# Kernel tuning notes

Hardware: AMD Instinct MI355X
Metric: run time of the kernel (lower is better)

## Reference

```python
import jax, jax.numpy as jnp
import numpy as np
import math

B, T, N, DS, A = 8, 64, 16, 128, 32
C, H, L = 1024, 16, 8
BLOCK = 64
MAX_TS = 1024


def _ln(x, w, b, eps=1e-5):
    m = x.mean(-1, keepdims=True)
    v = ((x - m) ** 2).mean(-1, keepdims=True)
    return (x - m) / jnp.sqrt(v + eps) * w + b


def _gelu(x):
    # tanh-approx GELU exactly as in the torch module
    return 0.5 * x * (1.0 + jnp.tanh(math.sqrt(2.0 / math.pi) * (x + 0.044715 * x ** 3)))


def setup_inputs() -> dict:
    key = jax.random.key(0)
    ks = jax.random.split(key, 24)
    w = lambda k, shape: (jax.random.normal(k, shape, jnp.float32) * 0.02)
    inp = {
        "states": jax.random.normal(ks[0], (B, T, N, DS), jnp.float32),
        "actions": jax.random.normal(ks[1], (B, T, N, A), jnp.float32),
        "timesteps": jax.random.randint(ks[2], (B, T), 0, MAX_TS),
        "pos_emb": w(ks[3], (2 * BLOCK, C)),
        "global_pos_emb": w(ks[4], (MAX_TS + 1, C)),
        "se_W": w(ks[5], (DS, C)), "se_b": jnp.zeros((C,), jnp.float32),
        "ae_W": w(ks[6], (A, C)), "ae_b": jnp.zeros((C,), jnp.float32),
        "ln1_w": jnp.ones((L, C), jnp.float32), "ln1_b": jnp.zeros((L, C), jnp.float32),
        "Wq": w(ks[7], (L, C, C)), "bq": jnp.zeros((L, C), jnp.float32),
        "Wk": w(ks[8], (L, C, C)), "bk": jnp.zeros((L, C), jnp.float32),
        "Wv": w(ks[9], (L, C, C)), "bv": jnp.zeros((L, C), jnp.float32),
        "Wp": w(ks[10], (L, C, C)), "bp": jnp.zeros((L, C), jnp.float32),
        "ln2_w": jnp.ones((L, C), jnp.float32), "ln2_b": jnp.zeros((L, C), jnp.float32),
        "W1": w(ks[11], (L, C, 4 * C)), "b1": jnp.zeros((L, 4 * C), jnp.float32),
        "W2": w(ks[12], (L, 4 * C, C)), "b2": jnp.zeros((L, C), jnp.float32),
        "lnf_w": jnp.ones((C,), jnp.float32), "lnf_b": jnp.zeros((C,), jnp.float32),
        "head_W": w(ks[13], (C, A)),
    }
    return inp


def _forward(states, actions, timesteps, pos_emb, global_pos_emb, se_W, se_b, ae_W, ae_b,
             ln1_w, ln1_b, Wq, bq, Wk, bk, Wv, bv, Wp, bp, ln2_w, ln2_b,
             W1, b1, W2, b2, lnf_w, lnf_b, head_W):
    BN = B * N
    S = 2 * T
    d = C // H
    st = states.transpose(0, 2, 1, 3).reshape(BN, T, DS)
    ac = actions.transpose(0, 2, 1, 3).reshape(BN, T, A)
    ts = jnp.broadcast_to(timesteps[:, None, :], (B, N, T)).reshape(BN, T)

    se = st @ se_W + se_b            # [BN, T, C]
    ae = ac @ ae_W + ae_b            # [BN, T, C]
    tok = jnp.stack([se, ae], axis=2).reshape(BN, S, C)  # interleave s,a

    gpe = global_pos_emb[ts]                              # [BN, T, C]
    pos = pos_emb[:S] + jnp.repeat(gpe, 2, axis=1)        # [BN, S, C]
    x = tok + pos

    causal = jnp.tril(jnp.ones((S, S), dtype=bool))

    def block(x, p):
        l1w, l1b, wq, bq_, wk, bk_, wv, bv_, wp, bp_, l2w, l2b, w1, b1_, w2, b2_ = p
        h = _ln(x, l1w, l1b)
        q = (h @ wq + bq_).reshape(BN, S, H, d).transpose(0, 2, 1, 3)
        k = (h @ wk + bk_).reshape(BN, S, H, d).transpose(0, 2, 1, 3)
        v = (h @ wv + bv_).reshape(BN, S, H, d).transpose(0, 2, 1, 3)
        att = jnp.einsum('bhqd,bhkd->bhqk', q, k) * (1.0 / math.sqrt(d))
        att = jnp.where(causal, att, -jnp.inf)
        att = jax.nn.softmax(att, axis=-1)
        y = jnp.einsum('bhqk,bhkd->bhqd', att, v).transpose(0, 2, 1, 3).reshape(BN, S, C)
        x = x + y @ wp + bp_
        h2 = _ln(x, l2w, l2b)
        x = x + _gelu(h2 @ w1 + b1_) @ w2 + b2_
        return x, None

    x, _ = jax.lax.scan(block, x, (ln1_w, ln1_b, Wq, bq, Wk, bk, Wv, bv, Wp, bp,
                                   ln2_w, ln2_b, W1, b1, W2, b2))
    x = _ln(x, lnf_w, lnf_b)
    logits = x @ head_W                                   # [BN, S, A]
    preds = logits[:, -2, :].reshape(B, N, A)
    return preds[:, None, :, :]                           # [B, 1, N, A]


def reference(states, actions, timesteps, pos_emb, global_pos_emb, se_W, se_b, ae_W, ae_b,
              ln1_w, ln1_b, Wq, bq, Wk, bk, Wv, bv, Wp, bp, ln2_w, ln2_b,
              W1, b1, W2, b2, lnf_w, lnf_b, head_W):
    return _forward(states, actions, timesteps, pos_emb, global_pos_emb, se_W, se_b, ae_W, ae_b,
                    ln1_w, ln1_b, Wq, bq, Wk, bk, Wv, bv, Wp, bp, ln2_w, ln2_b,
                    W1, b1, W2, b2, lnf_w, lnf_b, head_W)
```

## Files before the change

### kernel.cpp

```cpp
#include <hip/hip_runtime.h>
#include <math.h>


typedef float  float4v __attribute__((ext_vector_type(4)));
typedef short  short8  __attribute__((ext_vector_type(8)));

__device__ inline unsigned short f2b(float f) {
    unsigned int u = __float_as_uint(f);
    u += 0x7fffu + ((u >> 16) & 1u);
    return (unsigned short)(u >> 16);
}
__device__ inline float gelu_f(float v) {
    return 0.5f * v * (1.0f + tanhf(0.7978845608028654f * (v + 0.044715f * v * v * v)));
}
__device__ inline float4v mfma16(short8 a, short8 b, float4v c) {
    return __builtin_amdgcn_mfma_f32_16x16x32_bf16(a, b, c, 0, 0, 0);
}
#define GLOAD_LDS16(gp, lp)                                                 \
    __builtin_amdgcn_global_load_lds(                                       \
        (__attribute__((address_space(1))) void*)(gp),                      \
        (__attribute__((address_space(3))) void*)(lp), 16, 0, 0)

__global__ __launch_bounds__(256) void embed_kernel(
    const float* __restrict__ states, const float* __restrict__ actions,
    const int* __restrict__ timesteps, const float* __restrict__ pos_emb,
    const float* __restrict__ gpe_tab, const float* __restrict__ seW,
    const float* __restrict__ seb, const float* __restrict__ aeW,
    const float* __restrict__ aeb, float* __restrict__ x)
{
    const int c0 = blockIdx.x * 128;
    const int m0 = blockIdx.y * 32;
    const int bn = m0 >> 7;
    const int b  = bn >> 4, n = bn & 15;
    const int s_base = m0 & 127;
    const int tid = threadIdx.x;

    __shared__ float st[16][128];
    __shared__ float ac[16][32];
    for (int idx = tid; idx < 16 * 128; idx += 256) {
        int rr = idx >> 7, ds = idx & 127;
        int t = (s_base >> 1) + rr;
        st[rr][ds] = states[(((size_t)b * 64 + t) * 16 + n) * 128 + ds];
    }
    for (int idx = tid; idx < 16 * 32; idx += 256) {
        int rr = idx >> 5, a = idx & 31;
        int t = (s_base >> 1) + rr;
        ac[rr][a] = actions[(((size_t)b * 64 + t) * 16 + n) * 32 + a];
    }
    __syncthreads();

    const int half = tid >> 7;
    const int sub  = tid & 127;
    const int cg   = sub & 31;
    const int rg   = sub >> 5;

    float acc[4][4];
    for (int i = 0; i < 4; i++) for (int j = 0; j < 4; j++) acc[i][j] = 0.f;

    if (half == 0) {
        for (int kk = 0; kk < 128; kk++) {
            float4 w4 = *(const float4*)&seW[(size_t)kk * 1024 + c0 + cg * 4];
            for (int r4 = 0; r4 < 4; r4++) {
                float sv = st[rg * 4 + r4][kk];
                acc[r4][0] += sv * w4.x; acc[r4][1] += sv * w4.y;
                acc[r4][2] += sv * w4.z; acc[r4][3] += sv * w4.w;
            }
        }
    } else {
        for (int kk = 0; kk < 32; kk++) {
            float4 w4 = *(const float4*)&aeW[(size_t)kk * 1024 + c0 + cg * 4];
            for (int r4 = 0; r4 < 4; r4++) {
                float sv = ac[rg * 4 + r4][kk];
                acc[r4][0] += sv * w4.x; acc[r4][1] += sv * w4.y;
                acc[r4][2] += sv * w4.z; acc[r4][3] += sv * w4.w;
            }
        }
    }
    const float* bias = half ? aeb : seb;
    float4 b4 = *(const float4*)&bias[c0 + cg * 4];
    for (int r4 = 0; r4 < 4; r4++) {
        int rr = rg * 4 + r4;
        int s  = s_base + rr * 2 + half;
        int t  = (s_base >> 1) + rr;
        int m  = bn * 128 + s;
        int ts = timesteps[b * 64 + t];
        float4 p4 = *(const float4*)&pos_emb[(size_t)s * 1024 + c0 + cg * 4];
        float4 g4 = *(const float4*)&gpe_tab[(size_t)ts * 1024 + c0 + cg * 4];
        float4 o;
        o.x = acc[r4][0] + b4.x + p4.x + g4.x;
        o.y = acc[r4][1] + b4.y + p4.y + g4.y;
        o.z = acc[r4][2] + b4.z + p4.z + g4.z;
        o.w = acc[r4][3] + b4.w + p4.w + g4.w;
        *(float4*)&x[(size_t)m * 1024 + c0 + cg * 4] = o;
    }
}

__global__ __launch_bounds__(256) void transpose_kernel(
    const float* __restrict__ src, unsigned short* __restrict__ dst, int K, int N)
{
    __shared__ float tile[32][65];
    const int n0 = blockIdx.x * 32, k0 = blockIdx.y * 64;
    const int tid = threadIdx.x;
    const int nl = tid & 31, kl = tid >> 5;
    for (int p = 0; p < 8; p++)
        tile[nl][p * 8 + kl] = src[(size_t)(k0 + p * 8 + kl) * N + n0 + nl];
    __syncthreads();
    const int n2 = tid >> 3, kseg = tid & 7;
    unsigned short o8[8];
    for (int u = 0; u < 8; u++) o8[u] = f2b(tile[n2][kseg * 8 + u]);
    *(uint4*)&dst[(size_t)(n0 + n2) * K + k0 + kseg * 8] = *(uint4*)o8;
}

__global__ __launch_bounds__(256) void ln_kernel(
    const float* __restrict__ x, const float* __restrict__ w,
    const float* __restrict__ b, unsigned short* __restrict__ out)
{
    const int tid = threadIdx.x;
    const int row = blockIdx.x * 2 + (tid >> 7);
    const int sub = tid & 127;
    const float* xr = x + (size_t)row * 1024 + sub * 8;
    float4 a = *(const float4*)xr;
    float4 c = *(const float4*)(xr + 4);
    float s  = a.x + a.y + a.z + a.w + c.x + c.y + c.z + c.w;
    float s2 = a.x*a.x + a.y*a.y + a.z*a.z + a.w*a.w
             + c.x*c.x + c.y*c.y + c.z*c.z + c.w*c.w;
    for (int o = 32; o > 0; o >>= 1) { s += __shfl_down(s, o); s2 += __shfl_down(s2, o); }
    __shared__ float ls[4], ls2[4];
    if ((tid & 63) == 0) { ls[tid >> 6] = s; ls2[tid >> 6] = s2; }
    __syncthreads();
    const int wp = (tid >> 7) * 2;
    s  = ls[wp] + ls[wp + 1];
    s2 = ls2[wp] + ls2[wp + 1];
    float mean = s * (1.f / 1024.f);
    float var  = s2 * (1.f / 1024.f) - mean * mean;
    float inv  = rsqrtf(var + 1e-5f);
    float4 wa = *(const float4*)&w[sub * 8];
    float4 wc = *(const float4*)&w[sub * 8 + 4];
    float4 ba = *(const float4*)&b[sub * 8];
    float4 bc = *(const float4*)&b[sub * 8 + 4];
    unsigned short o8[8];
    o8[0] = f2b((a.x - mean) * inv * wa.x + ba.x);
    o8[1] = f2b((a.y - mean) * inv * wa.y + ba.y);
    o8[2] = f2b((a.z - mean) * inv * wa.z + ba.z);
    o8[3] = f2b((a.w - mean) * inv * wa.w + ba.w);
    o8[4] = f2b((c.x - mean) * inv * wc.x + bc.x);
    o8[5] = f2b((c.y - mean) * inv * wc.y + bc.y);
    o8[6] = f2b((c.z - mean) * inv * wc.z + bc.z);
    o8[7] = f2b((c.w - mean) * inv * wc.w + bc.w);
    *(uint4*)&out[(size_t)row * 1024 + sub * 8] = *(uint4*)o8;
}

template <int MODE>
__global__ __launch_bounds__(256) void gemm_kernel(
    const unsigned short* __restrict__ A, const unsigned short* __restrict__ Bt,
    const float* __restrict__ bias, const float* __restrict__ resid,
    void* __restrict__ outp, int M, int N, int K)
{
    __shared__ unsigned short As[128][32];
    __shared__ unsigned short Bs[128][32];
    __shared__ __align__(16) char Osmem[32768];
    const int tid = threadIdx.x;
    const int w  = tid >> 6, l = tid & 63;
    const int wr = w >> 1, wc = w & 1;
    const int qd = l >> 4, r = l & 15;
    const int m0 = blockIdx.y * 128, n0 = blockIdx.x * 128;

    const unsigned short* Ab = A  + (size_t)m0 * K;
    const unsigned short* Bb = Bt + (size_t)n0 * K;

    float4v acc[4][4];
    float4v zero = {0.f, 0.f, 0.f, 0.f};
    for (int i = 0; i < 4; i++) for (int j = 0; j < 4; j++) acc[i][j] = zero;

    const int ra0 = tid >> 2,         ca0 = (tid & 3) * 8;
    const int ra1 = (tid + 256) >> 2, ca1 = ((tid + 256) & 3) * 8;

    for (int k0 = 0; k0 < K; k0 += 32) {
        GLOAD_LDS16(Ab + (size_t)ra0 * K + k0 + ca0, &As[ra0][ca0]);
        GLOAD_LDS16(Ab + (size_t)ra1 * K + k0 + ca1, &As[ra1][ca1]);
        GLOAD_LDS16(Bb + (size_t)ra0 * K + k0 + ca0, &Bs[ra0][ca0]);
        GLOAD_LDS16(Bb + (size_t)ra1 * K + k0 + ca1, &Bs[ra1][ca1]);
        __syncthreads();
        short8 af[4], bfv[4];
        for (int i = 0; i < 4; i++) af[i]  = *(const short8*)&As[wr * 64 + i * 16 + r][qd * 8];
        for (int j = 0; j < 4; j++) bfv[j] = *(const short8*)&Bs[wc * 64 + j * 16 + r][qd * 8];
        for (int i = 0; i < 4; i++)
            for (int j = 0; j < 4; j++)
                acc[i][j] = mfma16(af[i], bfv[j], acc[i][j]);
        __syncthreads();
    }

    if (MODE != 2) {
        unsigned short (*Ob)[128] = (unsigned short (*)[128])Osmem;
        for (int i = 0; i < 4; i++) {
            const int rl = wr * 64 + i * 16 + qd * 4;
            for (int j = 0; j < 4; j++) {
                const int cl = wc * 64 + j * 16 + r;
                const float bv = bias[n0 + cl];
                for (int t4 = 0; t4 < 4; t4++) {
                    float v = acc[i][j][t4] + bv;
                    if (MODE == 1) v = gelu_f(v);
                    Ob[rl + t4][cl] = f2b(v);
                }
            }
        }
        __syncthreads();
        unsigned short* op = (unsigned short*)outp;
        for (int it = 0; it < 8; it++) {
            const int idx = it * 256 + tid;
            const int rl = idx >> 4, seg = idx & 15;
            *(uint4*)&op[(size_t)(m0 + rl) * N + n0 + seg * 8] = *(uint4*)&Ob[rl][seg * 8];
        }
    } else {
        float (*Of)[128] = (float (*)[128])Osmem;
        float* op = (float*)outp;
        for (int p = 0; p < 2; p++) {
            if (wr == p) {
                for (int i = 0; i < 4; i++) {
                    const int rl = i * 16 + qd * 4;
                    for (int j = 0; j < 4; j++) {
                        const int cl = wc * 64 + j * 16 + r;
                        const float bv = bias[n0 + cl];
                        for (int t4 = 0; t4 < 4; t4++)
                            Of[rl + t4][cl] = acc[i][j][t4] + bv;
                    }
                }
            }
            __syncthreads();
            for (int it = 0; it < 8; it++) {
                const int idx = it * 256 + tid;
                const int rl = idx >> 5, c4 = (idx & 31) * 4;
                const size_t go = (size_t)(m0 + p * 64 + rl) * N + n0 + c4;
                float4 rv = *(const float4*)&resid[go];
                float4 ov = *(float4*)&Of[rl][c4];
                ov.x += rv.x; ov.y += rv.y; ov.z += rv.z; ov.w += rv.w;
                *(float4*)&op[go] = ov;
            }
            __syncthreads();
        }
    }
}

__global__ __launch_bounds__(256) void attn_kernel(
    const unsigned short* __restrict__ qm, const unsigned short* __restrict__ km,
    const unsigned short* __restrict__ vm, unsigned short* __restrict__ ym)
{
    const int bn = blockIdx.x >> 4, hd = blockIdx.x & 15;
    __shared__ unsigned short QK[2][128][64];
    __shared__ unsigned short Vt[64][128];
    __shared__ float Sc[128][128];
    __shared__ float rsum[128];
    unsigned short (*Pb)[128] = (unsigned short (*)[128])QK;

    const int tid = threadIdx.x;
    const int w = tid >> 6, l = tid & 63, qd = l >> 4, r = l & 15;
    const size_t base = ((size_t)bn * 128) * 1024 + hd * 64;

    for (int idx = tid; idx < 1024; idx += 256) {
        int row = idx >> 3, seg = idx & 7;
        *(uint4*)&QK[0][row][seg * 8] = *(const uint4*)&qm[base + (size_t)row * 1024 + seg * 8];
        *(uint4*)&QK[1][row][seg * 8] = *(const uint4*)&km[base + (size_t)row * 1024 + seg * 8];
    }
    for (int idx = tid; idx < 8192; idx += 256) {
        int s = idx >> 6, d = idx & 63;
        Vt[d][s] = vm[base + (size_t)s * 1024 + d];
    }
    __syncthreads();

    for (int im = 0; im < 2; im++) {
        const int i = w * 2 + im;
        float4v acc[8];
        float4v zero = {0.f, 0.f, 0.f, 0.f};
        for (int j = 0; j < 8; j++) acc[j] = zero;
        for (int k0 = 0; k0 < 64; k0 += 32) {
            short8 af = *(const short8*)&QK[0][i * 16 + r][k0 + qd * 8];
            for (int j = 0; j < 8; j++) {
                short8 bf = *(const short8*)&QK[1][j * 16 + r][k0 + qd * 8];
                acc[j] = mfma16(af, bf, acc[j]);
            }
        }
        for (int j = 0; j < 8; j++)
            for (int t4 = 0; t4 < 4; t4++)
                Sc[i * 16 + qd * 4 + t4][j * 16 + r] = acc[j][t4] * 0.125f;
    }
    __syncthreads();

    if (tid < 128) {
        const int s = tid;
        float mx = -1e30f;
        for (int j = 0; j <= s; j++) mx = fmaxf(mx, Sc[s][j]);
        float sum = 0.f;
        for (int j = 0; j <= s; j++) {
            float e = __expf(Sc[s][j] - mx);
            sum += e;
            Pb[s][j] = f2b(e);
        }
        for (int j = s + 1; j < 128; j++) Pb[s][j] = 0;
        rsum[s] = 1.f / sum;
    }
    __syncthreads();

    float4v acc2[2][4];
    {
        float4v zero = {0.f, 0.f, 0.f, 0.f};
        for (int im = 0; im < 2; im++) for (int j = 0; j < 4; j++) acc2[im][j] = zero;
    }
    for (int im = 0; im < 2; im++) {
        const int i = w * 2 + im;
        for (int k0 = 0; k0 < 128; k0 += 32) {
            short8 af = *(const short8*)&Pb[i * 16 + r][k0 + qd * 8];
            for (int j = 0; j < 4; j++) {
                short8 bf = *(const short8*)&Vt[j * 16 + r][k0 + qd * 8];
                acc2[im][j] = mfma16(af, bf, acc2[im][j]);
            }
        }
    }
    __syncthreads();
    unsigned short (*Ys)[64] = (unsigned short (*)[64])Vt;
    for (int im = 0; im < 2; im++) {
        const int i = w * 2 + im;
        for (int j = 0; j < 4; j++)
            for (int t4 = 0; t4 < 4; t4++) {
                const int srow = i * 16 + qd * 4 + t4;
                Ys[srow][j * 16 + r] = f2b(acc2[im][j][t4] * rsum[srow]);
            }
    }
    __syncthreads();
    for (int it = 0; it < 4; it++) {
        const int idx = it * 256 + tid;
        const int row = idx >> 3, seg = idx & 7;
        *(uint4*)&ym[base + (size_t)row * 1024 + seg * 8] = *(uint4*)&Ys[row][seg * 8];
    }
}

__global__ __launch_bounds__(256) void final_kernel(
    const float* __restrict__ x, const float* __restrict__ lnw,
    const float* __restrict__ lnb, const float* __restrict__ headW,
    float* __restrict__ out)
{
    const int bn = blockIdx.x;
    const int tid = threadIdx.x;
    const float* xr = x + ((size_t)bn * 128 + 126) * 1024;
    float4 v = *(const float4*)&xr[tid * 4];
    float s  = v.x + v.y + v.z + v.w;
    float s2 = v.x * v.x + v.y * v.y + v.z * v.z + v.w * v.w;
    for (int o = 32; o > 0; o >>= 1) { s += __shfl_down(s, o); s2 += __shfl_down(s2, o); }
    __shared__ float ls[4], ls2[4];
    if ((tid & 63) == 0) { ls[tid >> 6] = s; ls2[tid >> 6] = s2; }
    __syncthreads();
    s  = ls[0] + ls[1] + ls[2] + ls[3];
    s2 = ls2[0] + ls2[1] + ls2[2] + ls2[3];
    float mean = s * (1.f / 1024.f);
    float var  = s2 * (1.f / 1024.f) - mean * mean;
    float inv  = rsqrtf(var + 1e-5f);
    __shared__ float hf[1024];
    float4 wv = *(const float4*)&lnw[tid * 4];
    float4 bv = *(const float4*)&lnb[tid * 4];
    hf[tid * 4 + 0] = (v.x - mean) * inv * wv.x + bv.x;
    hf[tid * 4 + 1] = (v.y - mean) * inv * wv.y + bv.y;
    hf[tid * 4 + 2] = (v.z - mean) * inv * wv.z + bv.z;
    hf[tid * 4 + 3] = (v.w - mean) * inv * wv.w + bv.w;
    __syncthreads();
    const int a = tid & 31, part = tid >> 5;
    float sum = 0.f;
    for (int c = part * 128; c < (part + 1) * 128; c++)
        sum += hf[c] * headW[(size_t)c * 32 + a];
    __shared__ float red[256];
    red[tid] = sum;
    __syncthreads();
    if (part == 0) {
        float tot = 0.f;
        for (int p = 0; p < 8; p++) tot += red[p * 32 + a];
        out[(size_t)bn * 32 + a] = tot;
    }
}

extern "C" void kernel_launch(void* const* d_in, const int* in_sizes, int n_in,
                              void* d_out, int out_size, void* d_ws, size_t ws_size,
                              hipStream_t stream)
{
    const float* states    = (const float*)d_in[0];
    const float* actions   = (const float*)d_in[1];
    const int*   timesteps = (const int*)  d_in[2];
    const float* pos_emb   = (const float*)d_in[3];
    const float* gpe_tab   = (const float*)d_in[4];
    const float* seW  = (const float*)d_in[5];
    const float* seb  = (const float*)d_in[6];
    const float* aeW  = (const float*)d_in[7];
    const float* aeb  = (const float*)d_in[8];
    const float* ln1w = (const float*)d_in[9];
    const float* ln1b = (const float*)d_in[10];
    const float* Wq = (const float*)d_in[11];
    const float* bq = (const float*)d_in[12];
    const float* Wk = (const float*)d_in[13];
    const float* bk = (const float*)d_in[14];
    const float* Wv = (const float*)d_in[15];
    const float* bv = (const float*)d_in[16];
    const float* Wp = (const float*)d_in[17];
    const float* bp = (const float*)d_in[18];
    const float* ln2w = (const float*)d_in[19];
    const float* ln2b = (const float*)d_in[20];
    const float* W1 = (const float*)d_in[21];
    const float* b1 = (const float*)d_in[22];
    const float* W2 = (const float*)d_in[23];
    const float* b2 = (const float*)d_in[24];
    const float* lnfw  = (const float*)d_in[25];
    const float* lnfb  = (const float*)d_in[26];
    const float* headW = (const float*)d_in[27];

    char* ws = (char*)d_ws;
    const size_t MB = 1024 * 1024;
    float*          x   = (float*)ws;
    unsigned short* h   = (unsigned short*)(ws + 64 * MB);
    unsigned short* qb  = (unsigned short*)(ws + 96 * MB);
    unsigned short* kb  = (unsigned short*)(ws + 128 * MB);
    unsigned short* vb  = (unsigned short*)(ws + 160 * MB);
    unsigned short* yb  = (unsigned short*)(ws + 192 * MB);
    unsigned short* ub  = (unsigned short*)(ws + 96 * MB);
    unsigned short* wqT = (unsigned short*)(ws + 224 * MB);
    unsigned short* wkT = (unsigned short*)(ws + 226 * MB);
    unsigned short* wvT = (unsigned short*)(ws + 228 * MB);
    unsigned short* wpT = (unsigned short*)(ws + 230 * MB);
    unsigned short* w1T = (unsigned short*)(ws + 232 * MB);
    unsigned short* w2T = (unsigned short*)(ws + 240 * MB);

    embed_kernel<<<dim3(8, 512), 256, 0, stream>>>(
        states, actions, timesteps, pos_emb, gpe_tab, seW, seb, aeW, aeb, x);

    for (int lyr = 0; lyr < 8; lyr++) {
        const size_t oC  = (size_t)lyr * 1024 * 1024;
        const size_t oC4 = (size_t)lyr * 1024 * 4096;
        transpose_kernel<<<dim3(32, 16),  256, 0, stream>>>(Wq + oC,  wqT, 1024, 1024);
        transpose_kernel<<<dim3(32, 16),  256, 0, stream>>>(Wk + oC,  wkT, 1024, 1024);
        transpose_kernel<<<dim3(32, 16),  256, 0, stream>>>(Wv + oC,  wvT, 1024, 1024);
        transpose_kernel<<<dim3(32, 16),  256, 0, stream>>>(Wp + oC,  wpT, 1024, 1024);
        transpose_kernel<<<dim3(128, 16), 256, 0, stream>>>(W1 + oC4, w1T, 1024, 4096);
        transpose_kernel<<<dim3(32, 64),  256, 0, stream>>>(W2 + oC4, w2T, 4096, 1024);

        ln_kernel<<<8192, 256, 0, stream>>>(x, ln1w + lyr * 1024, ln1b + lyr * 1024, h);
        gemm_kernel<0><<<dim3(8, 128), 256, 0, stream>>>(h, wqT, bq + lyr * 1024, nullptr, qb, 16384, 1024, 1024);
        gemm_kernel<0><<<dim3(8, 128), 256, 0, stream>>>(h, wkT, bk + lyr * 1024, nullptr, kb, 16384, 1024, 1024);
        gemm_kernel<0><<<dim3(8, 128), 256, 0, stream>>>(h, wvT, bv + lyr * 1024, nullptr, vb, 16384, 1024, 1024);
        attn_kernel<<<2048, 256, 0, stream>>>(qb, kb, vb, yb);
        gemm_kernel<2><<<dim3(8, 128), 256, 0, stream>>>(yb, wpT, bp + lyr * 1024, x, x, 16384, 1024, 1024);
        ln_kernel<<<8192, 256, 0, stream>>>(x, ln2w + lyr * 1024, ln2b + lyr * 1024, h);
        gemm_kernel<1><<<dim3(32, 128), 256, 0, stream>>>(h, w1T, b1 + lyr * 4096, nullptr, ub, 16384, 4096, 1024);
        gemm_kernel<2><<<dim3(8, 128), 256, 0, stream>>>(ub, w2T, b2 + lyr * 1024, x, x, 16384, 1024, 4096);
    }

    final_kernel<<<128, 256, 0, stream>>>(x, lnfw, lnfb, headW, (float*)d_out);
}
```

Baseline: 7.753 ms.

## Prune last layer to needed rows, swizzle LDS, parallelize attention softmax

In the final layer only row 126 of each sequence feeds the output, so the projection, LN2 and MLP GEMMs now run on those 128 rows via strided views instead of all 16384 rows. GEMM and attention kernels gain XOR-swizzled shared-memory layouts to cut bank conflicts. The attention softmax now uses all 256 threads with vectorized reads, and the V transpose goes through LDS with vector loads. GELU is rewritten in an exp-based sigmoid form that is algebraically equivalent to the tanh version. The main risks are the added index arithmetic and the strided last-layer launches being correct.

```diff
diff --git a/kernel.cpp b/kernel.cpp
--- a/kernel.cpp
+++ b/kernel.cpp
@@ -11,7 +11,8 @@
     return (unsigned short)(u >> 16);
 }
 __device__ inline float gelu_f(float v) {
-    return 0.5f * v * (1.0f + tanhf(0.7978845608028654f * (v + 0.044715f * v * v * v)));
+    float z2 = 1.5957691216057308f * v + 0.07135481282377437f * v * v * v;
+    return v - v / (__expf(z2) + 1.0f);
 }
 __device__ inline float4v mfma16(short8 a, short8 b, float4v c) {
     return __builtin_amdgcn_mfma_f32_16x16x32_bf16(a, b, c, 0, 0, 0);
@@ -112,13 +113,13 @@
 }
 
 __global__ __launch_bounds__(256) void ln_kernel(
-    const float* __restrict__ x, const float* __restrict__ w,
+    const float* __restrict__ x, long xrs, const float* __restrict__ w,
     const float* __restrict__ b, unsigned short* __restrict__ out)
 {
     const int tid = threadIdx.x;
     const int row = blockIdx.x * 2 + (tid >> 7);
     const int sub = tid & 127;
-    const float* xr = x + (size_t)row * 1024 + sub * 8;
+    const float* xr = x + (size_t)row * xrs + sub * 8;
     float4 a = *(const float4*)xr;
     float4 c = *(const float4*)(xr + 4);
     float s  = a.x + a.y + a.z + a.w + c.x + c.y + c.z + c.w;
@@ -154,36 +155,36 @@
 __global__ __launch_bounds__(256) void gemm_kernel(
     const unsigned short* __restrict__ A, const unsigned short* __restrict__ Bt,
     const float* __restrict__ bias, const float* __restrict__ resid,
-    void* __restrict__ outp, int M, int N, int K)
-{
-    __shared__ unsigned short As[128][32];
-    __shared__ unsigned short Bs[128][32];
-    __shared__ __align__(16) char Osmem[32768];
+    void* __restrict__ outp, int N, int K, long Ars, long Ors)
+{
+    __shared__ __align__(16) char smem[32768];
+    unsigned short* As = (unsigned short*)smem;
+    unsigned short* Bs = (unsigned short*)(smem + 16384);
     const int tid = threadIdx.x;
     const int w  = tid >> 6, l = tid & 63;
     const int wr = w >> 1, wc = w & 1;
     const int qd = l >> 4, r = l & 15;
     const int m0 = blockIdx.y * 128, n0 = blockIdx.x * 128;
 
-    const unsigned short* Ab = A  + (size_t)m0 * K;
+    const unsigned short* Ab = A  + (size_t)m0 * Ars;
     const unsigned short* Bb = Bt + (size_t)n0 * K;
 
     float4v acc[4][4];
     float4v zero = {0.f, 0.f, 0.f, 0.f};
     for (int i = 0; i < 4; i++) for (int j = 0; j < 4; j++) acc[i][j] = zero;
 
-    const int ra0 = tid >> 2,         ca0 = (tid & 3) * 8;
-    const int ra1 = (tid + 256) >> 2, ca1 = ((tid + 256) & 3) * 8;
+    const int ra0 = tid >> 2,  ca = (tid & 3) * 8;
+    const int ra1 = ra0 + 64;
 
     for (int k0 = 0; k0 < K; k0 += 32) {
-        GLOAD_LDS16(Ab + (size_t)ra0 * K + k0 + ca0, &As[ra0][ca0]);
-        GLOAD_LDS16(Ab + (size_t)ra1 * K + k0 + ca1, &As[ra1][ca1]);
-        GLOAD_LDS16(Bb + (size_t)ra0 * K + k0 + ca0, &Bs[ra0][ca0]);
-        GLOAD_LDS16(Bb + (size_t)ra1 * K + k0 + ca1, &Bs[ra1][ca1]);
+        GLOAD_LDS16(Ab + (size_t)ra0 * Ars + k0 + ca, As + tid * 8);
+        GLOAD_LDS16(Ab + (size_t)ra1 * Ars + k0 + ca, As + (256 + tid) * 8);
+        GLOAD_LDS16(Bb + (size_t)ra0 * K   + k0 + ca, Bs + tid * 8);
+        GLOAD_LDS16(Bb + (size_t)ra1 * K   + k0 + ca, Bs + (256 + tid) * 8);
         __syncthreads();
         short8 af[4], bfv[4];
-        for (int i = 0; i < 4; i++) af[i]  = *(const short8*)&As[wr * 64 + i * 16 + r][qd * 8];
-        for (int j = 0; j < 4; j++) bfv[j] = *(const short8*)&Bs[wc * 64 + j * 16 + r][qd * 8];
+        for (int i = 0; i < 4; i++) af[i]  = *(const short8*)(As + (wr*64 + i*16 + r)*32 + qd*8);
+        for (int j = 0; j < 4; j++) bfv[j] = *(const short8*)(Bs + (wc*64 + j*16 + r)*32 + qd*8);
         for (int i = 0; i < 4; i++)
             for (int j = 0; j < 4; j++)
                 acc[i][j] = mfma16(af[i], bfv[j], acc[i][j]);
@@ -191,16 +192,16 @@
     }
 
     if (MODE != 2) {
-        unsigned short (*Ob)[128] = (unsigned short (*)[128])Osmem;
+        unsigned short* Ob = (unsigned short*)smem;
         for (int i = 0; i < 4; i++) {
-            const int rl = wr * 64 + i * 16 + qd * 4;
             for (int j = 0; j < 4; j++) {
                 const int cl = wc * 64 + j * 16 + r;
                 const float bv = bias[n0 + cl];
                 for (int t4 = 0; t4 < 4; t4++) {
+                    const int rl = wr * 64 + i * 16 + qd * 4 + t4;
                     float v = acc[i][j][t4] + bv;
                     if (MODE == 1) v = gelu_f(v);
-                    Ob[rl + t4][cl] = f2b(v);
+                    Ob[rl * 128 + (((cl >> 3) ^ (rl & 15)) << 3) + (cl & 7)] = f2b(v);
                 }
             }
         }
@@ -209,30 +210,33 @@
         for (int it = 0; it < 8; it++) {
             const int idx = it * 256 + tid;
             const int rl = idx >> 4, seg = idx & 15;
-            *(uint4*)&op[(size_t)(m0 + rl) * N + n0 + seg * 8] = *(uint4*)&Ob[rl][seg * 8];
+            *(uint4*)&op[(size_t)(m0 + rl) * Ors + n0 + seg * 8] =
+                *(uint4*)&Ob[rl * 128 + ((seg ^ (rl & 15)) << 3)];
         }
     } else {
-        float (*Of)[128] = (float (*)[128])Osmem;
+        float* Of = (float*)smem;
         float* op = (float*)outp;
         for (int p = 0; p < 2; p++) {
             if (wr == p) {
                 for (int i = 0; i < 4; i++) {
-                    const int rl = i * 16 + qd * 4;
                     for (int j = 0; j < 4; j++) {
                         const int cl = wc * 64 + j * 16 + r;
                         const float bv = bias[n0 + cl];
-                        for (int t4 = 0; t4 < 4; t4++)
-                            Of[rl + t4][cl] = acc[i][j][t4] + bv;
+                        for (int t4 = 0; t4 < 4; t4++) {
+                            const int lr = i * 16 + qd * 4 + t4;
+                            Of[lr * 128 + (((cl >> 2) ^ (lr & 31)) << 2) + (cl & 3)] =
+                                acc[i][j][t4] + bv;
+                        }
                     }
                 }
             }
             __syncthreads();
             for (int it = 0; it < 8; it++) {
                 const int idx = it * 256 + tid;
-                const int rl = idx >> 5, c4 = (idx & 31) * 4;
-                const size_t go = (size_t)(m0 + p * 64 + rl) * N + n0 + c4;
+                const int lr = idx >> 5, c4 = idx & 31;
+                const size_t go = (size_t)(m0 + p * 64 + lr) * Ors + n0 + c4 * 4;
                 float4 rv = *(const float4*)&resid[go];
-                float4 ov = *(float4*)&Of[rl][c4];
+                float4 ov = *(const float4*)&Of[lr * 128 + ((c4 ^ (lr & 31)) << 2)];
                 ov.x += rv.x; ov.y += rv.y; ov.z += rv.z; ov.w += rv.w;
                 *(float4*)&op[go] = ov;
             }
@@ -246,90 +250,139 @@
     const unsigned short* __restrict__ vm, unsigned short* __restrict__ ym)
 {
     const int bn = blockIdx.x >> 4, hd = blockIdx.x & 15;
-    __shared__ unsigned short QK[2][128][64];
-    __shared__ unsigned short Vt[64][128];
-    __shared__ float Sc[128][128];
-    __shared__ float rsum[128];
-    unsigned short (*Pb)[128] = (unsigned short (*)[128])QK;
+    __shared__ __align__(16) unsigned short QK[2][128 * 64];
+    __shared__ __align__(16) unsigned short Vt[64 * 128];
+    __shared__ __align__(16) float Sc[128 * 128];
+    __shared__ float pmax[2][128], psum[2][128], rsum[128];
 
     const int tid = threadIdx.x;
     const int w = tid >> 6, l = tid & 63, qd = l >> 4, r = l & 15;
-    const size_t base = ((size_t)bn * 128) * 1024 + hd * 64;
-
+    const size_t base = ((size_t)bn * 128) * 1024 + (size_t)hd * 64;
+
+    unsigned short* Vs = (unsigned short*)Sc;
     for (int idx = tid; idx < 1024; idx += 256) {
         int row = idx >> 3, seg = idx & 7;
-        *(uint4*)&QK[0][row][seg * 8] = *(const uint4*)&qm[base + (size_t)row * 1024 + seg * 8];
-        *(uint4*)&QK[1][row][seg * 8] = *(const uint4*)&km[base + (size_t)row * 1024 + seg * 8];
-    }
-    for (int idx = tid; idx < 8192; idx += 256) {
-        int s = idx >> 6, d = idx & 63;
-        Vt[d][s] = vm[base + (size_t)s * 1024 + d];
-    }
-    __syncthreads();
-
+        int sw = (seg ^ (row & 7)) << 3;
+        *(uint4*)&QK[0][row * 64 + sw] = *(const uint4*)&qm[base + (size_t)row * 1024 + seg * 8];
+        *(uint4*)&QK[1][row * 64 + sw] = *(const uint4*)&km[base + (size_t)row * 1024 + seg * 8];
+        *(uint4*)&Vs[row * 64 + seg * 8] = *(const uint4*)&vm[base + (size_t)row * 1024 + seg * 8];
+    }
+    __syncthreads();
+
+    for (int idx = tid; idx < 1024; idx += 256) {
+        int d = idx & 63, sg = idx >> 6;
+        unsigned short tmp[8];
+        for (int u = 0; u < 8; u++) tmp[u] = Vs[(sg * 8 + u) * 64 + d];
+        *(uint4*)&Vt[d * 128 + ((sg ^ (d & 15)) << 3)] = *(uint4*)tmp;
+    }
+
+    float4v accS[2][8];
+    { float4v z = {0,0,0,0}; for (int a = 0; a < 2; a++) for (int j = 0; j < 8; j++) accS[a][j] = z; }
     for (int im = 0; im < 2; im++) {
         const int i = w * 2 + im;
-        float4v acc[8];
-        float4v zero = {0.f, 0.f, 0.f, 0.f};
-        for (int j = 0; j < 8; j++) acc[j] = zero;
+        const int rowA = i * 16 + r;
         for (int k0 = 0; k0 < 64; k0 += 32) {
-            short8 af = *(const short8*)&QK[0][i * 16 + r][k0 + qd * 8];
+            short8 af = *(const short8*)&QK[0][rowA * 64 + ((((k0 >> 3) + qd) ^ (rowA & 7)) << 3)];
             for (int j = 0; j < 8; j++) {
-                short8 bf = *(const short8*)&QK[1][j * 16 + r][k0 + qd * 8];
-                acc[j] = mfma16(af, bf, acc[j]);
-            }
-        }
-        for (int j = 0; j < 8; j++)
-            for (int t4 = 0; t4 < 4; t4++)
-                Sc[i * 16 + qd * 4 + t4][j * 16 + r] = acc[j][t4] * 0.125f;
-    }
-    __syncthreads();
-
-    if (tid < 128) {
-        const int s = tid;
-        float mx = -1e30f;
-        for (int j = 0; j <= s; j++) mx = fmaxf(mx, Sc[s][j]);
-        float sum = 0.f;
-        for (int j = 0; j <= s; j++) {
-            float e = __expf(Sc[s][j] - mx);
-            sum += e;
-            Pb[s][j] = f2b(e);
-        }
-        for (int j = s + 1; j < 128; j++) Pb[s][j] = 0;
-        rsum[s] = 1.f / sum;
-    }
-    __syncthreads();
-
-    float4v acc2[2][4];
-    {
-        float4v zero = {0.f, 0.f, 0.f, 0.f};
-        for (int im = 0; im < 2; im++) for (int j = 0; j < 4; j++) acc2[im][j] = zero;
-    }
+                const int rowB = j * 16 + r;
+                short8 bf = *(const short8*)&QK[1][rowB * 64 + ((((k0 >> 3) + qd) ^ (rowB & 7)) << 3)];
+                accS[im][j] = mfma16(af, bf, accS[im][j]);
+            }
+        }
+    }
+    __syncthreads();
+
     for (int im = 0; im < 2; im++) {
         const int i = w * 2 + im;
+        for (int j = 0; j < 8; j++)
+            for (int t4 = 0; t4 < 4; t4++) {
+                const int row = i * 16 + qd * 4 + t4;
+                const int col = j * 16 + r;
+                Sc[row * 128 + (((col >> 2) ^ (row & 31)) << 2) + (col & 3)] =
+                    accS[im][j][t4] * 0.125f;
+            }
+    }
+    __syncthreads();
+
+    {
+        const int s = tid & 127, half = tid >> 7;
+        float mx = -1e30f;
+        for (int g = half * 16; g < half * 16 + 16; g++) {
+            if (4 * g > s) break;
+            float4 v4 = *(const float4*)&Sc[s * 128 + ((g ^ (s & 31)) << 2)];
+            mx = fmaxf(mx, v4.x);
+            if (4 * g + 1 <= s) mx = fmaxf(mx, v4.y);
+            if (4 * g + 2 <= s) mx = fmaxf(mx, v4.z);
+            if (4 * g + 3 <= s) mx = fmaxf(mx, v4.w);
+        }
+        pmax[half][s] = mx;
+    }
+    __syncthreads();
+    {
+        const int s = tid & 127, half = tid >> 7;
+        const float mx = fmaxf(pmax[0][s], pmax[1][s]);
+        unsigned short* Pb = &QK[0][0];
+        float sum = 0.f;
+        for (int gg = half * 8; gg < half * 8 + 8; gg++) {
+            unsigned short o8[8] = {0, 0, 0, 0, 0, 0, 0, 0};
+            const int c0 = gg * 8;
+            if (c0 <= s) {
+                float4 a4 = *(const float4*)&Sc[s * 128 + (((2 * gg) ^ (s & 31)) << 2)];
+                float4 b4 = *(const float4*)&Sc[s * 128 + (((2 * gg + 1) ^ (s & 31)) << 2)];
+                float e;
+                e = __expf(a4.x - mx);                sum += e; o8[0] = f2b(e);
+                if (c0 + 1 <= s) { e = __expf(a4.y - mx); sum += e; o8[1] = f2b(e); }
+                if (c0 + 2 <= s) { e = __expf(a4.z - mx); sum += e; o8[2] = f2b(e); }
+                if (c0 + 3 <= s) { e = __expf(a4.w - mx); sum += e; o8[3] = f2b(e); }
+                if (c0 + 4 <= s) { e = __expf(b4.x - mx); sum += e; o8[4] = f2b(e); }
+                if (c0 + 5 <= s) { e = __expf(b4.y - mx); sum += e; o8[5] = f2b(e); }
+                if (c0 + 6 <= s) { e = __expf(b4.z - mx); sum += e; o8[6] = f2b(e); }
+                if (c0 + 7 <= s) { e = __expf(b4.w - mx); sum += e; o8[7] = f2b(e); }
+            }
+            *(uint4*)&Pb[s * 128 + ((gg ^ (s & 15)) << 3)] = *(uint4*)o8;
+        }
+        psum[half][s] = sum;
+    }
+    __syncthreads();
+    if (tid < 128) rsum[tid] = 1.f / (psum[0][tid] + psum[1][tid]);
+
+    const unsigned short* Pb = &QK[0][0];
+    float4v accO[2][4];
+    { float4v z = {0,0,0,0}; for (int a = 0; a < 2; a++) for (int j = 0; j < 4; j++) accO[a][j] = z; }
+    for (int im = 0; im < 2; im++) {
+        const int i = w * 2 + im;
+        const int rowA = i * 16 + r;
         for (int k0 = 0; k0 < 128; k0 += 32) {
-            short8 af = *(const short8*)&Pb[i * 16 + r][k0 + qd * 8];
+            short8 af = *(const short8*)&Pb[rowA * 128 + ((((k0 >> 3) + qd) ^ (rowA & 15)) << 3)];
             for (int j = 0; j < 4; j++) {
-                short8 bf = *(const short8*)&Vt[j * 16 + r][k0 + qd * 8];
-                acc2[im][j] = mfma16(af, bf, acc2[im][j]);
-            }
-        }
-    }
-    __syncthreads();
-    unsigned short (*Ys)[64] = (unsigned short (*)[64])Vt;
+                const int rowB = j * 16 + r;
+                short8 bf = *(const short8*)&Vt[rowB * 128 + ((((k0 >> 3) + qd) ^ (rowB & 15)) << 3)];
+                accO[im][j] = mfma16(af, bf, accO[im][j]);
+            }
+        }
+    }
+    __syncthreads();
+
+    float* Ys = Sc;
     for (int im = 0; im < 2; im++) {
         const int i = w * 2 + im;
         for (int j = 0; j < 4; j++)
             for (int t4 = 0; t4 < 4; t4++) {
-                const int srow = i * 16 + qd * 4 + t4;
-                Ys[srow][j * 16 + r] = f2b(acc2[im][j][t4] * rsum[srow]);
-            }
-    }
-    __syncthreads();
-    for (int it = 0; it < 4; it++) {
-        const int idx = it * 256 + tid;
-        const int row = idx >> 3, seg = idx & 7;
-        *(uint4*)&ym[base + (size_t)row * 1024 + seg * 8] = *(uint4*)&Ys[row][seg * 8];
+                const int row = i * 16 + qd * 4 + t4;
+                const int col = j * 16 + r;
+                Ys[row * 64 + (((col >> 2) ^ (row & 15)) << 2) + (col & 3)] =
+                    accO[im][j][t4] * rsum[row];
+            }
+    }
+    __syncthreads();
+    for (int idx = tid; idx < 1024; idx += 256) {
+        const int row = idx >> 3, gg = idx & 7;
+        float4 a4 = *(const float4*)&Ys[row * 64 + (((2 * gg) ^ (row & 15)) << 2)];
+        float4 b4 = *(const float4*)&Ys[row * 64 + (((2 * gg + 1) ^ (row & 15)) << 2)];
+        unsigned short o8[8];
+        o8[0] = f2b(a4.x); o8[1] = f2b(a4.y); o8[2] = f2b(a4.z); o8[3] = f2b(a4.w);
+        o8[4] = f2b(b4.x); o8[5] = f2b(b4.y); o8[6] = f2b(b4.z); o8[7] = f2b(b4.w);
+        *(uint4*)&ym[base + (size_t)row * 1024 + gg * 8] = *(uint4*)o8;
     }
 }
 
@@ -427,7 +480,11 @@
     embed_kernel<<<dim3(8, 512), 256, 0, stream>>>(
         states, actions, timesteps, pos_emb, gpe_tab, seW, seb, aeW, aeb, x);
 
+    const long G = 128L * 1024L;
+    float* xg = x + 126 * 1024;
+
     for (int lyr = 0; lyr < 8; lyr++) {
+        const bool last = (lyr == 7);
         const size_t oC  = (size_t)lyr * 1024 * 1024;
         const size_t oC4 = (size_t)lyr * 1024 * 4096;
         transpose_kernel<<<dim3(32, 16),  256, 0, stream>>>(Wq + oC,  wqT, 1024, 1024);
@@ -437,15 +494,23 @@
         transpose_kernel<<<dim3(128, 16), 256, 0, stream>>>(W1 + oC4, w1T, 1024, 4096);
         transpose_kernel<<<dim3(32, 64),  256, 0, stream>>>(W2 + oC4, w2T, 4096, 1024);
 
-        ln_kernel<<<8192, 256, 0, stream>>>(x, ln1w + lyr * 1024, ln1b + lyr * 1024, h);
-        gemm_kernel<0><<<dim3(8, 128), 256, 0, stream>>>(h, wqT, bq + lyr * 1024, nullptr, qb, 16384, 1024, 1024);
-        gemm_kernel<0><<<dim3(8, 128), 256, 0, stream>>>(h, wkT, bk + lyr * 1024, nullptr, kb, 16384, 1024, 1024);
-        gemm_kernel<0><<<dim3(8, 128), 256, 0, stream>>>(h, wvT, bv + lyr * 1024, nullptr, vb, 16384, 1024, 1024);
+        ln_kernel<<<8192, 256, 0, stream>>>(x, 1024L, ln1w + lyr * 1024, ln1b + lyr * 1024, h);
+        gemm_kernel<0><<<dim3(8, 128), 256, 0, stream>>>(h, wqT, bq + lyr * 1024, nullptr, qb, 1024, 1024, 1024L, 1024L);
+        gemm_kernel<0><<<dim3(8, 128), 256, 0, stream>>>(h, wkT, bk + lyr * 1024, nullptr, kb, 1024, 1024, 1024L, 1024L);
+        gemm_kernel<0><<<dim3(8, 128), 256, 0, stream>>>(h, wvT, bv + lyr * 1024, nullptr, vb, 1024, 1024, 1024L, 1024L);
         attn_kernel<<<2048, 256, 0, stream>>>(qb, kb, vb, yb);
-        gemm_kernel<2><<<dim3(8, 128), 256, 0, stream>>>(yb, wpT, bp + lyr * 1024, x, x, 16384, 1024, 1024);
-        ln_kernel<<<8192, 256, 0, stream>>>(x, ln2w + lyr * 1024, ln2b + lyr * 1024, h);
-        gemm_kernel<1><<<dim3(32, 128), 256, 0, stream>>>(h, w1T, b1 + lyr * 4096, nullptr, ub, 16384, 4096, 1024);
-        gemm_kernel<2><<<dim3(8, 128), 256, 0, stream>>>(ub, w2T, b2 + lyr * 1024, x, x, 16384, 1024, 4096);
+
+        if (!last) {
+            gemm_kernel<2><<<dim3(8, 128), 256, 0, stream>>>(yb, wpT, bp + lyr * 1024, x, x, 1024, 1024, 1024L, 1024L);
+            ln_kernel<<<8192, 256, 0, stream>>>(x, 1024L, ln2w + lyr * 1024, ln2b + lyr * 1024, h);
+            gemm_kernel<1><<<dim3(32, 128), 256, 0, stream>>>(h, w1T, b1 + lyr * 4096, nullptr, ub, 4096, 1024, 1024L, 4096L);
+            gemm_kernel<2><<<dim3(8, 128), 256, 0, stream>>>(ub, w2T, b2 + lyr * 1024, x, x, 1024, 4096, 4096L, 1024L);
+        } else {
+            gemm_kernel<2><<<dim3(8, 1), 256, 0, stream>>>(yb + 126 * 1024, wpT, bp + lyr * 1024, xg, xg, 1024, 1024, G, G);
+            ln_kernel<<<64, 256, 0, stream>>>(xg, G, ln2w + lyr * 1024, ln2b + lyr * 1024, h);
+            gemm_kernel<1><<<dim3(32, 1), 256, 0, stream>>>(h, w1T, b1 + lyr * 4096, nullptr, ub, 4096, 1024, 1024L, 4096L);
+            gemm_kernel<2><<<dim3(8, 1), 256, 0, stream>>>(ub, w2T, b2 + lyr * 1024, xg, xg, 1024, 4096, 4096L, G);
+        }
     }
 
     final_kernel<<<128, 256, 0, stream>>>(x, lnfw, lnfb, headW, (float*)d_out);
```

Result: faster. 6.825 ms (-12.0%).
